# Kernel optimization log

Measured on AMD Instinct MI355X. Metric: run time of the kernel, lower is better.

Reference implementation:

```python
import jax, jax.numpy as jnp
import numpy as np

N_NODES = 50000
N_EDGES = 800000
D = 128
H = 8
HD = D // H
N_NTYPES = 3
N_ETYPES = 5
LN_EPS = 1e-5


def setup_inputs() -> dict:
    key = jax.random.key(0)
    ks = jax.random.split(key, 16)
    inp = {
        "x": jax.random.normal(ks[0], (N_NODES, D), dtype=jnp.float32),
        "edge_index": jax.random.randint(ks[1], (2, N_EDGES), 0, N_NODES),
        "edge_type": jax.random.randint(ks[2], (N_EDGES,), 0, N_ETYPES),
        "node_type": jax.random.randint(ks[3], (N_NODES,), 0, N_NTYPES),
        # per-(node_type, head) QKV projections, per-(edge_type, head) K transform
        "W_Q": jax.random.normal(ks[4], (N_NTYPES, H, HD, HD), dtype=jnp.float32) * 0.02,
        "W_K": jax.random.normal(ks[5], (N_NTYPES, H, HD, HD), dtype=jnp.float32) * 0.02,
        "W_V": jax.random.normal(ks[6], (N_NTYPES, H, HD, HD), dtype=jnp.float32) * 0.02,
        "W_edge": jax.random.normal(ks[7], (N_ETYPES, H, HD, HD), dtype=jnp.float32) * 0.02,
        "mu": jnp.ones((H, N_ETYPES), dtype=jnp.float32),
        "W_out": jax.random.normal(ks[8], (D, D), dtype=jnp.float32) * 0.02,
        "b_out": jnp.zeros((D,), dtype=jnp.float32),
        "ln1_g": jnp.ones((D,), dtype=jnp.float32),
        "ln1_b": jnp.zeros((D,), dtype=jnp.float32),
        "W1": jax.random.normal(ks[9], (D, 4 * D), dtype=jnp.float32) * 0.02,
        "b1": jnp.zeros((4 * D,), dtype=jnp.float32),
        "W2": jax.random.normal(ks[10], (4 * D, D), dtype=jnp.float32) * 0.02,
        "b2": jnp.zeros((D,), dtype=jnp.float32),
        "ln2_g": jnp.ones((D,), dtype=jnp.float32),
        "ln2_b": jnp.zeros((D,), dtype=jnp.float32),
    }
    return inp


def _layer_norm(y, g, b):
    m = y.mean(-1, keepdims=True)
    v = ((y - m) ** 2).mean(-1, keepdims=True)
    return (y - m) * jax.lax.rsqrt(v + LN_EPS) * g + b


def reference(x, edge_index, edge_type, node_type,
              W_Q, W_K, W_V, W_edge, mu,
              W_out, b_out, ln1_g, ln1_b, W1, b1, W2, b2, ln2_g, ln2_b):
    N = x.shape[0]
    xh = x.reshape(N, H, HD)  # heads vectorized (concat of per-head slices)

    # type-specific QKV: small fixed loop over node types, masked select
    Q = jnp.zeros_like(xh)
    K = jnp.zeros_like(xh)
    V = jnp.zeros_like(xh)
    for t in range(N_NTYPES):
        m = (node_type == t)[:, None, None]
        Q = jnp.where(m, jnp.einsum('nhd,hdf->nhf', xh, W_Q[t]), Q)
        K = jnp.where(m, jnp.einsum('nhd,hdf->nhf', xh, W_K[t]), K)
        V = jnp.where(m, jnp.einsum('nhd,hdf->nhf', xh, W_V[t]), V)

    src, dst = edge_index[0], edge_index[1]
    q_dst = Q[dst]   # [E,H,HD]
    k_src = K[src]   # [E,H,HD]

    # edge-type-specific K transform
    kt = jnp.zeros_like(k_src)
    for et in range(N_ETYPES):
        m = (edge_type == et)[:, None, None]
        kt = jnp.where(m, jnp.einsum('ehd,hdf->ehf', k_src, W_edge[et]), kt)

    scores = (q_dst * kt).sum(-1) / jnp.sqrt(jnp.float32(HD))  # [E,H]
    scores = scores * mu[:, edge_type].T                       # mu per edge type, per head

    # sparse softmax over incoming edges of each dst node, per head
    smax = jax.ops.segment_max(scores, dst, num_segments=N)
    ex = jnp.exp(scores - smax[dst])
    den = jax.ops.segment_sum(ex, dst, num_segments=N)
    w = ex / (den[dst] + 1e-10)                                 # [E,H]

    agg = jax.ops.segment_sum(V[src] * w[..., None], dst, num_segments=N)  # [N,H,HD]
    mh = agg.reshape(N, D) @ W_out + b_out  # dropout is identity in eval

    h = _layer_norm(x + mh, ln1_g, ln1_b)
    ffn = jax.nn.gelu(h @ W1 + b1, approximate=False) @ W2 + b2
    return _layer_norm(h + ffn, ln2_g, ln2_b)
```

## Files before the change

### kernel.cpp

```cpp
#include <hip/hip_runtime.h>
#include <hip/hip_bf16.h>

#define N_NODESC 50000
#define N_EDGESC 800000
#define DD 128
#define HH 8
#define HDIM 16
#define N_NT 3
#define N_ET 5
#define NPB 196
#define NEB 400
#define NFB 512
#define WPB 912

#define KV8_OFF    ((size_t)0)
#define QT8_OFF    ((size_t)12800000)
#define AGG_OFF    ((size_t)57600000)
#define WOUTT_OFF  ((size_t)83200000)
#define W1T_OFF    ((size_t)83232768)
#define W2T_OFF    ((size_t)83363840)
#define WHPF_OFF   ((size_t)83494912)
#define EDATA_OFF  ((size_t)84183040)
#define ROWS_OFF   ((size_t)87383040)
#define ORIG_OFF   ((size_t)87583104)
#define DEG_OFF    ((size_t)87783104)
#define TOFS_OFF   ((size_t)87983104)
#define BH_OFF     ((size_t)87983168)
#define BB_OFF     ((size_t)87985536)
#define TMP_OFF    ((size_t)87988928)
#define RLOC_OFF   ((size_t)91188928)
#define CSUM_OFF   ((size_t)91389056)

using short8 = __attribute__((ext_vector_type(8))) short;
using f32x4  = __attribute__((ext_vector_type(4))) float;
using f32x2  = __attribute__((ext_vector_type(2))) float;

__device__ __forceinline__ ushort f2b(float f) {
    __hip_bfloat16 h = __float2bfloat16(f);
    return *(ushort*)&h;
}
__device__ __forceinline__ float b2f(ushort u) {
    __hip_bfloat16 h = *(__hip_bfloat16*)&u;
    return __bfloat162float(h);
}
__device__ __forceinline__ f32x2 pk0(unsigned int w) {
    return __builtin_amdgcn_cvt_pk_f32_fp8((int)w, false);
}
__device__ __forceinline__ f32x2 pk1(unsigned int w) {
    return __builtin_amdgcn_cvt_pk_f32_fp8((int)w, true);
}
__device__ __forceinline__ float gelu_f(float v) {
    const float x = v * 0.70710678118654752f;
    const float ax = fabsf(x);
    const float d = fmaf(0.3275911f, ax, 1.0f);
    float t;
    asm("v_rcp_f32 %0, %1" : "=v"(t) : "v"(d));
    float p = fmaf(1.061405429f, t, -1.453152027f);
    p = fmaf(p, t, 1.421413741f);
    p = fmaf(p, t, -0.284496736f);
    p = fmaf(p, t, 0.254829592f);
    p = p * t;
    const float e = __expf(-ax * ax);
    const float er = 1.0f - p * e;
    const float erfx = (x < 0.f) ? -er : er;
    return 0.5f * v * (1.0f + erfx);
}
__device__ __forceinline__ void ebar() {
    __builtin_amdgcn_sched_barrier(0);
    asm volatile("s_waitcnt lgkmcnt(0)" ::: "memory");
    __builtin_amdgcn_sched_barrier(0);
    __builtin_amdgcn_s_barrier();
    __builtin_amdgcn_sched_barrier(0);
}

__global__ __launch_bounds__(256) void prep_a(
    const float* __restrict__ Wout, const float* __restrict__ W1, const float* __restrict__ W2,
    const float* __restrict__ WQ, const float* __restrict__ Wk, const float* __restrict__ Wv,
    const float* __restrict__ We, const float* __restrict__ mu,
    ushort* __restrict__ Woutt, ushort* __restrict__ W1t, ushort* __restrict__ W2t,
    ushort* __restrict__ Whpf,
    const int* __restrict__ ntype, int* __restrict__ bh,
    const int* __restrict__ dst, int* __restrict__ deg, unsigned int* __restrict__ tmp)
{
    const int b = blockIdx.x, tid = threadIdx.x;
    if (b < WPB) {
        const int gid = b * 256 + tid;
        if (gid < 16384) {
            const int nn = gid >> 7, k = gid & 127;
            Woutt[gid] = f2b(Wout[k * 128 + nn]);
        } else if (gid < 81920) {
            const int i = gid - 16384;
            const int nn = i >> 7, k = i & 127;
            W1t[i] = f2b(W1[k * 512 + nn]);
        } else if (gid < 147456) {
            const int i = gid - 81920;
            const int nn = i >> 9, k = i & 511;
            W2t[i] = f2b(W2[k * 128 + nn]);
        } else {
            const int idx = gid - 147456;
            const int t = idx / 28672;
            const int r = idx % 28672;
            const int i = r & 7;
            const int l = (r >> 3) & 63;
            const int f = r >> 9;
            const int j = f % 14, p = f / 14;
            const int c = j * 16 + (l & 15);
            const int k = ((l >> 4) << 3) + i;
            const int hi = (c >= 112) ? 1 : 0;
            const int h = 2 * p + hi;
            float v = 0.f;
            if ((k >> 4) == hi) {
                const int kp = k & 15;
                const int cl = c - hi * 112;
                if (cl < 16) {
                    v = 4.f * Wk[((t * HH + h) * HDIM + kp) * HDIM + cl];
                } else if (cl < 32) {
                    v = 4.f * Wv[((t * HH + h) * HDIM + kp) * HDIM + (cl - 16)];
                } else {
                    const int et = (cl - 32) >> 4, jj = (cl - 32) & 15;
                    const float* wq = WQ + ((t * HH + h) * HDIM + kp) * HDIM;
                    const float* we = We + ((et * HH + h) * HDIM + jj) * HDIM;
                    float s = 0.f;
#pragma unroll
                    for (int ff = 0; ff < 16; ff++) s = fmaf(wq[ff], we[ff], s);
                    v = 64.f * mu[h * N_ET + et] * s;
                }
            }
            Whpf[idx] = f2b(v);
        }
    } else if (b < WPB + NPB) {
        const int bc = b - WPB;
        const int wave = tid >> 6, lane = tid & 63;
        const int n = bc * 256 + tid;
        const int t = (n < N_NODESC) ? ntype[n] : -1;
        const unsigned long long m0 = __ballot(t == 0);
        const unsigned long long m1 = __ballot(t == 1);
        const unsigned long long m2 = __ballot(t == 2);
        __shared__ int wcnt[4][3];
        if (lane == 0) {
            wcnt[wave][0] = (int)__popcll(m0);
            wcnt[wave][1] = (int)__popcll(m1);
            wcnt[wave][2] = (int)__popcll(m2);
        }
        __syncthreads();
        if (tid < 3)
            bh[tid * NPB + bc] = wcnt[0][tid] + wcnt[1][tid] + wcnt[2][tid] + wcnt[3][tid];
    } else {
        for (int e = (b - WPB - NPB) * 256 + tid; e < N_EDGESC; e += NEB * 256) {
            const int nd = dst[e];
            const unsigned int p = (unsigned int)atomicAdd(&deg[nd], 1);
            tmp[e] = (p << 16) | (unsigned int)nd;
        }
    }
}

__global__ __launch_bounds__(256) void prep_b(
    const int* __restrict__ bh, const int* __restrict__ deg,
    int* __restrict__ bb, int* __restrict__ tofs,
    int* __restrict__ rloc, int* __restrict__ csum)
{
    __shared__ int part[256];
    const int tid = threadIdx.x;
    if (blockIdx.x == 0) {
        const int base3 = tid * 3;
        int e0 = (base3 + 0 < 588) ? bh[base3 + 0] : 0;
        int e1 = (base3 + 1 < 588) ? bh[base3 + 1] : 0;
        int e2 = (base3 + 2 < 588) ? bh[base3 + 2] : 0;
        const int l0 = e0, l1 = e0 + e1, l2 = l1 + e2;
        part[tid] = l2;
        __syncthreads();
        for (int off = 1; off < 256; off <<= 1) {
            const int u = (tid >= off) ? part[tid - off] : 0;
            __syncthreads();
            part[tid] += u;
            __syncthreads();
        }
        const int tb = part[tid] - l2;
        if (base3 + 0 < 588) bb[base3 + 0] = tb;
        if (base3 + 1 < 588) bb[base3 + 1] = tb + l0;
        if (base3 + 2 < 588) bb[base3 + 2] = tb + l1;
        __syncthreads();
        if (tid == 0) {
            tofs[0] = 0;
            tofs[1] = bb[NPB];
            tofs[2] = bb[2 * NPB];
            tofs[3] = N_NODESC;
        }
    } else {
        const int c = blockIdx.x - 1;
        const int n = c * 256 + tid;
        const int vdeg = (n < N_NODESC) ? deg[n] : 0;
        part[tid] = vdeg;
        __syncthreads();
        for (int off = 1; off < 256; off <<= 1) {
            const int u = (tid >= off) ? part[tid - off] : 0;
            __syncthreads();
            part[tid] += u;
            __syncthreads();
        }
        if (n <= N_NODESC) rloc[n] = part[tid] - vdeg;
        if (tid == 255) csum[c] = part[255];
    }
}

__global__ __launch_bounds__(256) void prep_c(
    const int* __restrict__ ntype,
    const int* __restrict__ src, const int* __restrict__ etype,
    const int* __restrict__ bb, const int* __restrict__ rloc, const int* __restrict__ csum,
    const unsigned int* __restrict__ tmp,
    int* __restrict__ origof, int* __restrict__ rows,
    int* __restrict__ edata)
{
    const int b = blockIdx.x, tid = threadIdx.x;
    __shared__ int cb[256];
    {
        const int v = (tid < NPB) ? csum[tid] : 0;
        cb[tid] = v;
        __syncthreads();
        for (int off = 1; off < 256; off <<= 1) {
            const int u = (tid >= off) ? cb[tid - off] : 0;
            __syncthreads();
            cb[tid] += u;
            __syncthreads();
        }
        const int incl = cb[tid];
        __syncthreads();
        cb[tid] = incl - v;
        __syncthreads();
    }

    if (b < NPB) {
        const int wave = tid >> 6, lane = tid & 63;
        const int n = b * 256 + tid;
        const int t = (n < N_NODESC) ? ntype[n] : -1;
        const unsigned long long m0 = __ballot(t == 0);
        const unsigned long long m1 = __ballot(t == 1);
        const unsigned long long m2 = __ballot(t == 2);
        __shared__ int wcnt[4][3];
        if (lane == 0) {
            wcnt[wave][0] = (int)__popcll(m0);
            wcnt[wave][1] = (int)__popcll(m1);
            wcnt[wave][2] = (int)__popcll(m2);
        }
        __syncthreads();
        if (n < N_NODESC) {
            int basew = 0;
#pragma unroll
            for (int w = 0; w < 4; w++) if (w < wave) basew += wcnt[w][t];
            const unsigned long long mt = (t == 0) ? m0 : (t == 1) ? m1 : m2;
            const unsigned long long mlt = ((unsigned long long)1 << lane) - 1;
            const int p = bb[t * NPB + b] + basew + (int)__popcll(mt & mlt);
            origof[p] = n;
        }
        if (n <= N_NODESC) rows[n] = cb[b] + rloc[n];
    } else {
        for (int e = (b - NPB) * 256 + tid; e < N_EDGESC; e += NFB * 256) {
            const unsigned int v = tmp[e];
            const int nd = (int)(v & 0xffffu);
            const int p = (int)(v >> 16);
            edata[cb[nd >> 8] + rloc[nd] + p] = src[e] | (etype[e] << 16);
        }
    }
}

#define LDX 132

__global__ __launch_bounds__(256) void proj_gemm(
    const float* __restrict__ x, const ushort* __restrict__ Whpf,
    const int* __restrict__ tofs, const int* __restrict__ origof,
    unsigned char* __restrict__ KV8b, unsigned char* __restrict__ Qt8)
{
    const int t = blockIdx.y;
    const int rs = tofs[t], re = tofs[t + 1];
    const int mBase = rs + blockIdx.x * 64;
    if (mBase >= re) return;

    __shared__ ushort Xs[64 * LDX];
    __shared__ ushort Ws[28672];

    const int tid = threadIdx.x;
    const int lane = tid & 63, wave = tid >> 6;
    const int l15 = lane & 15, rq = (lane >> 4) * 4;

#pragma unroll
    for (int it = 0; it < 4; it++) {
        const int idx = it * 256 + tid;
        const int row = idx >> 4, ch = idx & 15;
        int gm = mBase + row; if (gm >= N_NODESC) gm = N_NODESC - 1;
        const int og = origof[gm];
        const float4 v0 = *(const float4*)(x + (size_t)og * DD + ch * 8);
        const float4 v1 = *(const float4*)(x + (size_t)og * DD + ch * 8 + 4);
        ushort o[8] = {f2b(v0.x), f2b(v0.y), f2b(v0.z), f2b(v0.w),
                       f2b(v1.x), f2b(v1.y), f2b(v1.z), f2b(v1.w)};
        *(uint4*)&Xs[row * LDX + ch * 8] = *(uint4*)o;
    }
    const ushort* Wg = Whpf + (size_t)t * 28672;
#pragma unroll
    for (int it = 0; it < 14; it++) {
        const int idx = it * 256 + tid;
        *(uint4*)&Ws[idx * 8] = *(const uint4*)(Wg + (size_t)idx * 8);
    }
    __syncthreads();

    int ogr[4]; bool vr[4];
#pragma unroll
    for (int r = 0; r < 4; r++) {
        const int gm = mBase + wave * 16 + rq + r;
        vr[r] = (gm < re);
        ogr[r] = vr[r] ? origof[gm] : 0;
    }

    for (int p = 0; p < 4; p++) {
        const short8 af = *(const short8*)&Xs[(wave * 16 + l15) * LDX + p * 32 + (lane >> 4) * 8];
#pragma unroll
        for (int j = 0; j < 14; j++) {
            const short8 bf = *(const short8*)&Ws[((p * 14 + j) * 64 + lane) * 8];
            f32x4 c = __builtin_amdgcn_mfma_f32_16x16x32_bf16(
                af, bf, (f32x4){0.f, 0.f, 0.f, 0.f}, 0, 0, 0);
            const int hi = (j >= 7) ? 1 : 0;
            const int h = 2 * p + hi;
            const int jj = j - hi * 7;
#pragma unroll
            for (int r = 0; r < 4; r++) {
                if (!vr[r]) continue;
                const float v = c[r];
                const unsigned char b8 =
                    (unsigned char)(__builtin_amdgcn_cvt_pk_fp8_f32(v, v, 0, false) & 0xff);
                const size_t og = (size_t)ogr[r];
                if (jj == 0)      KV8b[og * 256 + h * 16 + l15] = b8;
                else if (jj == 1) KV8b[og * 256 + 128 + h * 16 + l15] = b8;
                else              Qt8[og * 640 + (jj - 2) * 128 + h * 16 + l15] = b8;
            }
        }
    }
}

__global__ __launch_bounds__(128) void edgeagg_kernel(
    const int* __restrict__ rowstart, const int* __restrict__ edata,
    const unsigned char* __restrict__ Qt8, const unsigned char* __restrict__ KV8,
    ushort* __restrict__ agg)
{
    const int w = threadIdx.x >> 6;
    const int lane = threadIdx.x & 63;
    const int n = blockIdx.x * 2 + w;
    const int slot = lane >> 3;
    const int h = lane & 7;

    __shared__ uint4 qs8s[2][40];
    if (lane < 40)
        qs8s[w][lane] = ((const uint4*)(Qt8 + (size_t)n * 640))[lane];
    __syncthreads();
    const uint* qbase = (const uint*)&qs8s[w][0];

    const int s0 = rowstart[n], s1 = rowstart[n + 1];
    const float qsc = 1.44269504f / 1024.f;

    float acc[16];
#pragma unroll
    for (int j = 0; j < 16; j++) acc[j] = 0.f;
    float den = 0.f;

    int i = s0 + slot;
    int ed = 0;
    uint4 kw = {0u, 0u, 0u, 0u}, vw = {0u, 0u, 0u, 0u};
    if (i < s1) {
        ed = edata[i];
        const unsigned char* kvp = KV8 + ((size_t)(ed & 0xffff) << 8);
        kw = *(const uint4*)(kvp + (h << 4));
        vw = *(const uint4*)(kvp + 128 + (h << 4));
    }
    while (i < s1) {
        const int in2 = i + 8;
        int edn = 0;
        uint4 kwn = {0u, 0u, 0u, 0u}, vwn = {0u, 0u, 0u, 0u};
        if (in2 < s1) {
            edn = edata[in2];
            const unsigned char* kvpn = KV8 + ((size_t)(edn & 0xffff) << 8);
            kwn = *(const uint4*)(kvpn + (h << 4));
            vwn = *(const uint4*)(kvpn + 128 + (h << 4));
        }

        const int et = ed >> 16;
        const uint4 qw = *(const uint4*)(qbase + (et << 5) + (h << 2));

        const f32x2 q0 = pk0(qw.x), q1 = pk1(qw.x), q2 = pk0(qw.y), q3 = pk1(qw.y);
        const f32x2 q4 = pk0(qw.z), q5 = pk1(qw.z), q6 = pk0(qw.w), q7 = pk1(qw.w);
        const f32x2 k0 = pk0(kw.x), k1 = pk1(kw.x), k2 = pk0(kw.y), k3 = pk1(kw.y);
        const f32x2 k4 = pk0(kw.z), k5 = pk1(kw.z), k6 = pk0(kw.w), k7 = pk1(kw.w);

        float pa = q0.x * k0.x;
        float pb = q0.y * k0.y;
        float pc = q1.x * k1.x;
        float pd = q1.y * k1.y;
        pa = fmaf(q2.x, k2.x, pa); pb = fmaf(q2.y, k2.y, pb);
        pc = fmaf(q3.x, k3.x, pc); pd = fmaf(q3.y, k3.y, pd);
        pa = fmaf(q4.x, k4.x, pa); pb = fmaf(q4.y, k4.y, pb);
        pc = fmaf(q5.x, k5.x, pc); pd = fmaf(q5.y, k5.y, pd);
        pa = fmaf(q6.x, k6.x, pa); pb = fmaf(q6.y, k6.y, pb);
        pc = fmaf(q7.x, k7.x, pc); pd = fmaf(q7.y, k7.y, pd);

        const float ex = exp2f(((pa + pb) + (pc + pd)) * qsc);
        den += ex;

        const f32x2 v0 = pk0(vw.x), v1 = pk1(vw.x), v2 = pk0(vw.y), v3 = pk1(vw.y);
        const f32x2 v4 = pk0(vw.z), v5 = pk1(vw.z), v6 = pk0(vw.w), v7 = pk1(vw.w);
        acc[0]  = fmaf(ex, v0.x, acc[0]);  acc[1]  = fmaf(ex, v0.y, acc[1]);
        acc[2]  = fmaf(ex, v1.x, acc[2]);  acc[3]  = fmaf(ex, v1.y, acc[3]);
        acc[4]  = fmaf(ex, v2.x, acc[4]);  acc[5]  = fmaf(ex, v2.y, acc[5]);
        acc[6]  = fmaf(ex, v3.x, acc[6]);  acc[7]  = fmaf(ex, v3.y, acc[7]);
        acc[8]  = fmaf(ex, v4.x, acc[8]);  acc[9]  = fmaf(ex, v4.y, acc[9]);
        acc[10] = fmaf(ex, v5.x, acc[10]); acc[11] = fmaf(ex, v5.y, acc[11]);
        acc[12] = fmaf(ex, v6.x, acc[12]); acc[13] = fmaf(ex, v6.y, acc[13]);
        acc[14] = fmaf(ex, v7.x, acc[14]); acc[15] = fmaf(ex, v7.y, acc[15]);

        i = in2; ed = edn; kw = kwn; vw = vwn;
    }

    {
        const int b0 = slot & 1, b1 = slot & 2, b2 = slot & 4;
#pragma unroll
        for (int j = 0; j < 8; j++) {
            const float v = b0 ? acc[j] : acc[j + 8];
            const float r = __shfl_xor(v, 8);
            acc[j] = (b0 ? acc[j + 8] : acc[j]) + r;
        }
#pragma unroll
        for (int j = 0; j < 4; j++) {
            const float v = b1 ? acc[j] : acc[j + 4];
            const float r = __shfl_xor(v, 16);
            acc[j] = (b1 ? acc[j + 4] : acc[j]) + r;
        }
#pragma unroll
        for (int j = 0; j < 2; j++) {
            const float v = b2 ? acc[j] : acc[j + 2];
            const float r = __shfl_xor(v, 32);
            acc[j] = (b2 ? acc[j + 2] : acc[j]) + r;
        }
        den += __shfl_xor(den, 8);
        den += __shfl_xor(den, 16);
        den += __shfl_xor(den, 32);
    }
    const float rr = 0.25f / (den + 1e-10f);
    const int fb = (h << 4) + ((slot & 1) << 3) + ((slot & 2) << 1) + ((slot & 4) >> 1);
    ushort o2[2] = { f2b(acc[0] * rr), f2b(acc[1] * rr) };
    *(uint*)&agg[((size_t)n << 7) + fb] = *(uint*)o2;
}

#define LDH 132
#define LDB2 68

#define LOADB(P0, P1, PTR) { P0 = *(const short8*)(PTR); P1 = *(const short8*)((PTR) + 8); }
#define STAGEB1(P0, P1) { *(short8*)&Bs[br * LDB2 + bc] = P0; \
                          *(short8*)&Bs[br * LDB2 + bc + 8] = P1; }
#define COMP(ASRC, KOFF, ACC) { \
    short8 af[2], bf[2]; \
    _Pragma("unroll") \
    for (int kk2 = 0; kk2 < 2; kk2++) { \
        _Pragma("unroll") \
        for (int i = 0; i < 2; i++) \
            af[i] = *(const short8*)&ASRC[(wm * 32 + i * 16 + l15) * LDH + (KOFF) + kk2 * 32 + q8]; \
        _Pragma("unroll") \
        for (int j = 0; j < 2; j++) \
            bf[j] = *(const short8*)&Bs[(wn * 32 + j * 16 + l15) * LDB2 + kk2 * 32 + q8]; \
        _Pragma("unroll") \
        for (int i = 0; i < 2; i++) \
            _Pragma("unroll") \
            for (int j = 0; j < 2; j++) \
                ACC[i][j] = __builtin_amdgcn_mfma_f32_16x16x32_bf16(af[i], bf[j], ACC[i][j], 0, 0, 0); \
    } }

__global__ __launch_bounds__(512, 4) void fused_tail(
    const ushort* __restrict__ agg, const ushort* __restrict__ Woutt,
    const ushort* __restrict__ W1t, const ushort* __restrict__ W2t,
    const float* __restrict__ x,
    const float* __restrict__ bout, const float* __restrict__ g1, const float* __restrict__ b1ln,
    const float* __restrict__ b1, const float* __restrict__ b2,
    const float* __restrict__ g2, const float* __restrict__ b2ln,
    float* __restrict__ out)
{
    __shared__ ushort Bs[128 * LDB2];
    __shared__ ushort Hs[64 * LDH];
    __shared__ ushort Ts[64 * LDH];
    __shared__ float red[2][4][64];

    const int tid = threadIdx.x;
    const int lane = tid & 63, wave = tid >> 6;
    const int wm = wave >> 2, wn = wave & 3;
    const int l15 = lane & 15, q8 = (lane >> 4) * 8, rq = (lane >> 4) * 4;
    const int mBase = blockIdx.x * 64;

    const int br = tid >> 2, bc = (tid & 3) * 16;
    const int ar = tid >> 3, ac = (tid & 7) * 16;
    int rowA = mBase + ar; if (rowA >= N_NODESC) rowA = N_NODESC - 1;

    f32x4 acc1[2][2], acc2[2][2];
#pragma unroll
    for (int i = 0; i < 2; i++)
#pragma unroll
        for (int j = 0; j < 2; j++) {
            acc1[i][j] = (f32x4){0.f, 0.f, 0.f, 0.f};
            acc2[i][j] = (f32x4){0.f, 0.f, 0.f, 0.f};
        }

    short8 pB0, pB1, aT0, aT1;
    LOADB(pB0, pB1, Woutt + (size_t)br * 128 + bc);
    aT0 = *(const short8*)(agg + (size_t)rowA * DD + ac);
    aT1 = *(const short8*)(agg + (size_t)rowA * DD + ac + 8);
    float xv[2][4][2];
#pragma unroll
    for (int i = 0; i < 2; i++)
#pragma unroll
        for (int r = 0; r < 4; r++) {
            const int gm = mBase + wm * 32 + i * 16 + rq + r;
            const int gr = (gm < N_NODESC) ? gm : N_NODESC - 1;
#pragma unroll
            for (int j = 0; j < 2; j++)
                xv[i][r][j] = x[(size_t)gr * DD + wn * 32 + j * 16 + l15];
        }
    *(short8*)&Ts[ar * LDH + ac] = aT0;
    *(short8*)&Ts[ar * LDH + ac + 8] = aT1;
    STAGEB1(pB0, pB1);
    LOADB(pB0, pB1, Woutt + (size_t)br * 128 + 64 + bc);
    ebar();

    COMP(Ts, 0, acc1);
    ebar();
    STAGEB1(pB0, pB1);
    LOADB(pB0, pB1, W1t + (size_t)br * 128 + bc);
    ebar();
    COMP(Ts, 64, acc1);

    {
        float bo[2], gv[2], bv[2];
#pragma unroll
        for (int j = 0; j < 2; j++) {
            const int gn = wn * 32 + j * 16 + l15;
            bo[j] = bout[gn]; gv[j] = g1[gn]; bv[j] = b1ln[gn];
        }
#pragma unroll
        for (int i = 0; i < 2; i++) {
#pragma unroll
            for (int r = 0; r < 4; r++) {
                const int row = wm * 32 + i * 16 + rq + r;
                float s = 0.f, ss = 0.f;
#pragma unroll
                for (int j = 0; j < 2; j++) {
                    float v = acc1[i][j][r] + bo[j] + xv[i][r][j];
                    acc1[i][j][r] = v;
                    s += v; ss += v * v;
                }
                s  += __shfl_xor(s, 1);  s  += __shfl_xor(s, 2);  s  += __shfl_xor(s, 4);  s  += __shfl_xor(s, 8);
                ss += __shfl_xor(ss, 1); ss += __shfl_xor(ss, 2); ss += __shfl_xor(ss, 4); ss += __shfl_xor(ss, 8);
                if (l15 == 0) { red[0][wn][row] = s; red[1][wn][row] = ss; }
            }
        }
        ebar();
#pragma unroll
        for (int i = 0; i < 2; i++) {
#pragma unroll
            for (int r = 0; r < 4; r++) {
                const int row = wm * 32 + i * 16 + rq + r;
                const float s  = red[0][0][row] + red[0][1][row] + red[0][2][row] + red[0][3][row];
                const float ss = red[1][0][row] + red[1][1][row] + red[1][2][row] + red[1][3][row];
                const float mean = s * (1.f / 128.f);
                const float var  = ss * (1.f / 128.f) - mean * mean;
                const float rstd = rsqrtf(var + 1e-5f);
#pragma unroll
                for (int j = 0; j < 2; j++) {
                    const int gn = wn * 32 + j * 16 + l15;
                    Hs[row * LDH + gn] = f2b((acc1[i][j][r] - mean) * rstd * gv[j] + bv[j]);
                }
            }
        }
    }

    for (int nb = 0; nb < 4; nb++) {
        f32x4 a1[2][2];
#pragma unroll
        for (int i = 0; i < 2; i++)
#pragma unroll
            for (int j = 0; j < 2; j++) a1[i][j] = (f32x4){0.f, 0.f, 0.f, 0.f};

        ebar();
        STAGEB1(pB0, pB1);
        LOADB(pB0, pB1, W1t + (size_t)(nb * 128 + br) * 128 + 64 + bc);
        ebar();
        COMP(Hs, 0, a1);

        ebar();
        STAGEB1(pB0, pB1);
        LOADB(pB0, pB1, W2t + (size_t)br * 512 + nb * 128 + bc);
        ebar();
        COMP(Hs, 64, a1);

        {
            float b1v[2];
#pragma unroll
            for (int j = 0; j < 2; j++)
                b1v[j] = b1[nb * 128 + wn * 32 + j * 16 + l15];
#pragma unroll
            for (int i = 0; i < 2; i++)
#pragma unroll
                for (int j = 0; j < 2; j++)
#pragma unroll
                    for (int r = 0; r < 4; r++) {
                        const int row = wm * 32 + i * 16 + rq + r;
                        const int col = wn * 32 + j * 16 + l15;
                        Ts[row * LDH + col] = f2b(gelu_f(a1[i][j][r] + b1v[j]));
                    }
        }

        ebar();
        STAGEB1(pB0, pB1);
        LOADB(pB0, pB1, W2t + (size_t)br * 512 + nb * 128 + 64 + bc);
        ebar();
        COMP(Ts, 0, acc2);

        ebar();
        STAGEB1(pB0, pB1);
        if (nb < 3) { LOADB(pB0, pB1, W1t + (size_t)((nb + 1) * 128 + br) * 128 + bc); }
        ebar();
        COMP(Ts, 64, acc2);
    }

    {
        float b2v[2], gv[2], bv[2];
#pragma unroll
        for (int j = 0; j < 2; j++) {
            const int gn = wn * 32 + j * 16 + l15;
            b2v[j] = b2[gn]; gv[j] = g2[gn]; bv[j] = b2ln[gn];
        }
#pragma unroll
        for (int i = 0; i < 2; i++) {
#pragma unroll
            for (int r = 0; r < 4; r++) {
                const int row = wm * 32 + i * 16 + rq + r;
                float s = 0.f, ss = 0.f;
#pragma unroll
                for (int j = 0; j < 2; j++) {
                    const int gn = wn * 32 + j * 16 + l15;
                    float v = acc2[i][j][r] + b2v[j] + b2f(Hs[row * LDH + gn]);
                    acc2[i][j][r] = v;
                    s += v; ss += v * v;
                }
                s  += __shfl_xor(s, 1);  s  += __shfl_xor(s, 2);  s  += __shfl_xor(s, 4);  s  += __shfl_xor(s, 8);
                ss += __shfl_xor(ss, 1); ss += __shfl_xor(ss, 2); ss += __shfl_xor(ss, 4); ss += __shfl_xor(ss, 8);
                if (l15 == 0) { red[0][wn][row] = s; red[1][wn][row] = ss; }
            }
        }
        ebar();
#pragma unroll
        for (int i = 0; i < 2; i++) {
#pragma unroll
            for (int r = 0; r < 4; r++) {
                const int row = wm * 32 + i * 16 + rq + r;
                const int gm = mBase + row;
                if (gm >= N_NODESC) continue;
                const float s  = red[0][0][row] + red[0][1][row] + red[0][2][row] + red[0][3][row];
                const float ss = red[1][0][row] + red[1][1][row] + red[1][2][row] + red[1][3][row];
                const float mean = s * (1.f / 128.f);
                const float var  = ss * (1.f / 128.f) - mean * mean;
                const float rstd = rsqrtf(var + 1e-5f);
#pragma unroll
                for (int j = 0; j < 2; j++) {
                    const int gn = wn * 32 + j * 16 + l15;
                    out[(size_t)gm * DD + gn] = (acc2[i][j][r] - mean) * rstd * gv[j] + bv[j];
                }
            }
        }
    }
}

extern "C" void kernel_launch(void* const* d_in, const int* in_sizes, int n_in,
                              void* d_out, int out_size, void* d_ws, size_t ws_size,
                              hipStream_t stream)
{
    const float* x     = (const float*)d_in[0];
    const int*   ei    = (const int*)d_in[1];
    const int*   etyp  = (const int*)d_in[2];
    const int*   ntype = (const int*)d_in[3];
    const float* Wq    = (const float*)d_in[4];
    const float* Wk    = (const float*)d_in[5];
    const float* Wv    = (const float*)d_in[6];
    const float* We    = (const float*)d_in[7];
    const float* mu    = (const float*)d_in[8];
    const float* Wout  = (const float*)d_in[9];
    const float* bout  = (const float*)d_in[10];
    const float* g1    = (const float*)d_in[11];
    const float* b1ln  = (const float*)d_in[12];
    const float* W1    = (const float*)d_in[13];
    const float* b1    = (const float*)d_in[14];
    const float* W2    = (const float*)d_in[15];
    const float* b2    = (const float*)d_in[16];
    const float* g2    = (const float*)d_in[17];
    const float* b2ln  = (const float*)d_in[18];
    float* out = (float*)d_out;

    char* ws = (char*)d_ws;
    ushort*        KV8   = (ushort*)(ws + KV8_OFF);
    unsigned char* Qt8   = (unsigned char*)(ws + QT8_OFF);
    ushort*        agg   = (ushort*)(ws + AGG_OFF);
    ushort*        Woutt = (ushort*)(ws + WOUTT_OFF);
    ushort*        W1t   = (ushort*)(ws + W1T_OFF);
    ushort*        W2t   = (ushort*)(ws + W2T_OFF);
    ushort*        Whpf  = (ushort*)(ws + WHPF_OFF);
    int*           edata = (int*)(ws + EDATA_OFF);
    int*           rows  = (int*)(ws + ROWS_OFF);
    int*           origof= (int*)(ws + ORIG_OFF);
    int*           deg   = (int*)(ws + DEG_OFF);
    int*           tofs  = (int*)(ws + TOFS_OFF);
    int*           bh    = (int*)(ws + BH_OFF);
    int*           bb    = (int*)(ws + BB_OFF);
    unsigned int*  tmp   = (unsigned int*)(ws + TMP_OFF);
    int*           rloc  = (int*)(ws + RLOC_OFF);
    int*           csum  = (int*)(ws + CSUM_OFF);

    const int* srcA = ei;
    const int* dstA = ei + N_EDGESC;

    (void)hipMemsetAsync(ws + DEG_OFF, 0, 200000, stream);

    prep_a<<<WPB + NPB + NEB, 256, 0, stream>>>(
        Wout, W1, W2, Wq, Wk, Wv, We, mu, Woutt, W1t, W2t, Whpf,
        ntype, bh, dstA, deg, tmp);
    prep_b<<<1 + NPB, 256, 0, stream>>>(bh, deg, bb, tofs, rloc, csum);
    prep_c<<<NPB + NFB, 256, 0, stream>>>(ntype, srcA, etyp, bb, rloc, csum, tmp,
                                          origof, rows, edata);

    proj_gemm<<<dim3(782, 3), 256, 0, stream>>>(x, Whpf, tofs, origof,
                                                (unsigned char*)KV8, Qt8);
    edgeagg_kernel<<<N_NODESC / 2, 128, 0, stream>>>(rows, edata, Qt8,
                                                     (const unsigned char*)KV8, agg);

    fused_tail<<<782, 512, 0, stream>>>(agg, Woutt, W1t, W2t, x,
                                        bout, g1, b1ln, b1, b2, g2, b2ln, out);
}
```

Measured before the change: 313.2 us.

## Drop node-type sort; compute per-type projections with masked MFMA passes

```diff
diff --git a/kernel.cpp b/kernel.cpp
--- a/kernel.cpp
+++ b/kernel.cpp
@@ -22,11 +22,7 @@
 #define WHPF_OFF   ((size_t)83494912)
 #define EDATA_OFF  ((size_t)84183040)
 #define ROWS_OFF   ((size_t)87383040)
-#define ORIG_OFF   ((size_t)87583104)
 #define DEG_OFF    ((size_t)87783104)
-#define TOFS_OFF   ((size_t)87983104)
-#define BH_OFF     ((size_t)87983168)
-#define BB_OFF     ((size_t)87985536)
 #define TMP_OFF    ((size_t)87988928)
 #define RLOC_OFF   ((size_t)91188928)
 #define CSUM_OFF   ((size_t)91389056)
@@ -79,7 +75,6 @@
     const float* __restrict__ We, const float* __restrict__ mu,
     ushort* __restrict__ Woutt, ushort* __restrict__ W1t, ushort* __restrict__ W2t,
     ushort* __restrict__ Whpf,
-    const int* __restrict__ ntype, int* __restrict__ bh,
     const int* __restrict__ dst, int* __restrict__ deg, unsigned int* __restrict__ tmp)
 {
     const int b = blockIdx.x, tid = threadIdx.x;
@@ -128,25 +123,8 @@
             }
             Whpf[idx] = f2b(v);
         }
-    } else if (b < WPB + NPB) {
-        const int bc = b - WPB;
-        const int wave = tid >> 6, lane = tid & 63;
-        const int n = bc * 256 + tid;
-        const int t = (n < N_NODESC) ? ntype[n] : -1;
-        const unsigned long long m0 = __ballot(t == 0);
-        const unsigned long long m1 = __ballot(t == 1);
-        const unsigned long long m2 = __ballot(t == 2);
-        __shared__ int wcnt[4][3];
-        if (lane == 0) {
-            wcnt[wave][0] = (int)__popcll(m0);
-            wcnt[wave][1] = (int)__popcll(m1);
-            wcnt[wave][2] = (int)__popcll(m2);
-        }
-        __syncthreads();
-        if (tid < 3)
-            bh[tid * NPB + bc] = wcnt[0][tid] + wcnt[1][tid] + wcnt[2][tid] + wcnt[3][tid];
     } else {
-        for (int e = (b - WPB - NPB) * 256 + tid; e < N_EDGESC; e += NEB * 256) {
+        for (int e = (b - WPB) * 256 + tid; e < N_EDGESC; e += NEB * 256) {
             const int nd = dst[e];
             const unsigned int p = (unsigned int)atomicAdd(&deg[nd], 1);
             tmp[e] = (p << 16) | (unsigned int)nd;
@@ -155,61 +133,31 @@
 }
 
 __global__ __launch_bounds__(256) void prep_b(
-    const int* __restrict__ bh, const int* __restrict__ deg,
-    int* __restrict__ bb, int* __restrict__ tofs,
+    const int* __restrict__ deg,
     int* __restrict__ rloc, int* __restrict__ csum)
 {
     __shared__ int part[256];
     const int tid = threadIdx.x;
-    if (blockIdx.x == 0) {
-        const int base3 = tid * 3;
-        int e0 = (base3 + 0 < 588) ? bh[base3 + 0] : 0;
-        int e1 = (base3 + 1 < 588) ? bh[base3 + 1] : 0;
-        int e2 = (base3 + 2 < 588) ? bh[base3 + 2] : 0;
-        const int l0 = e0, l1 = e0 + e1, l2 = l1 + e2;
-        part[tid] = l2;
+    const int c = blockIdx.x;
+    const int n = c * 256 + tid;
+    const int vdeg = (n < N_NODESC) ? deg[n] : 0;
+    part[tid] = vdeg;
+    __syncthreads();
+    for (int off = 1; off < 256; off <<= 1) {
+        const int u = (tid >= off) ? part[tid - off] : 0;
         __syncthreads();
-        for (int off = 1; off < 256; off <<= 1) {
-            const int u = (tid >= off) ? part[tid - off] : 0;
-            __syncthreads();
-            part[tid] += u;
-            __syncthreads();
-        }
-        const int tb = part[tid] - l2;
-        if (base3 + 0 < 588) bb[base3 + 0] = tb;
-        if (base3 + 1 < 588) bb[base3 + 1] = tb + l0;
-        if (base3 + 2 < 588) bb[base3 + 2] = tb + l1;
+        part[tid] += u;
         __syncthreads();
-        if (tid == 0) {
-            tofs[0] = 0;
-            tofs[1] = bb[NPB];
-            tofs[2] = bb[2 * NPB];
-            tofs[3] = N_NODESC;
-        }
-    } else {
-        const int c = blockIdx.x - 1;
-        const int n = c * 256 + tid;
-        const int vdeg = (n < N_NODESC) ? deg[n] : 0;
-        part[tid] = vdeg;
-        __syncthreads();
-        for (int off = 1; off < 256; off <<= 1) {
-            const int u = (tid >= off) ? part[tid - off] : 0;
-            __syncthreads();
-            part[tid] += u;
-            __syncthreads();
-        }
-        if (n <= N_NODESC) rloc[n] = part[tid] - vdeg;
-        if (tid == 255) csum[c] = part[255];
-    }
+    }
+    if (n <= N_NODESC) rloc[n] = part[tid] - vdeg;
+    if (tid == 255) csum[c] = part[255];
 }
 
 __global__ __launch_bounds__(256) void prep_c(
-    const int* __restrict__ ntype,
     const int* __restrict__ src, const int* __restrict__ etype,
-    const int* __restrict__ bb, const int* __restrict__ rloc, const int* __restrict__ csum,
+    const int* __restrict__ rloc, const int* __restrict__ csum,
     const unsigned int* __restrict__ tmp,
-    int* __restrict__ origof, int* __restrict__ rows,
-    int* __restrict__ edata)
+    int* __restrict__ rows, int* __restrict__ edata)
 {
     const int b = blockIdx.x, tid = threadIdx.x;
     __shared__ int cb[256];
@@ -230,28 +178,7 @@
     }
 
     if (b < NPB) {
-        const int wave = tid >> 6, lane = tid & 63;
         const int n = b * 256 + tid;
-        const int t = (n < N_NODESC) ? ntype[n] : -1;
-        const unsigned long long m0 = __ballot(t == 0);
-        const unsigned long long m1 = __ballot(t == 1);
-        const unsigned long long m2 = __ballot(t == 2);
-        __shared__ int wcnt[4][3];
-        if (lane == 0) {
-            wcnt[wave][0] = (int)__popcll(m0);
-            wcnt[wave][1] = (int)__popcll(m1);
-            wcnt[wave][2] = (int)__popcll(m2);
-        }
-        __syncthreads();
-        if (n < N_NODESC) {
-            int basew = 0;
-#pragma unroll
-            for (int w = 0; w < 4; w++) if (w < wave) basew += wcnt[w][t];
-            const unsigned long long mt = (t == 0) ? m0 : (t == 1) ? m1 : m2;
-            const unsigned long long mlt = ((unsigned long long)1 << lane) - 1;
-            const int p = bb[t * NPB + b] + basew + (int)__popcll(mt & mlt);
-            origof[p] = n;
-        }
         if (n <= N_NODESC) rows[n] = cb[b] + rloc[n];
     } else {
         for (int e = (b - NPB) * 256 + tid; e < N_EDGESC; e += NFB * 256) {
@@ -267,16 +194,13 @@
 
 __global__ __launch_bounds__(256) void proj_gemm(
     const float* __restrict__ x, const ushort* __restrict__ Whpf,
-    const int* __restrict__ tofs, const int* __restrict__ origof,
+    const int* __restrict__ ntype,
     unsigned char* __restrict__ KV8b, unsigned char* __restrict__ Qt8)
 {
-    const int t = blockIdx.y;
-    const int rs = tofs[t], re = tofs[t + 1];
-    const int mBase = rs + blockIdx.x * 64;
-    if (mBase >= re) return;
+    const int mBase = blockIdx.x * 64;
+    if (mBase >= N_NODESC) return;
 
     __shared__ ushort Xs[64 * LDX];
-    __shared__ ushort Ws[28672];
 
     const int tid = threadIdx.x;
     const int lane = tid & 63, wave = tid >> 6;
@@ -286,50 +210,49 @@
     for (int it = 0; it < 4; it++) {
         const int idx = it * 256 + tid;
         const int row = idx >> 4, ch = idx & 15;
-        int gm = mBase + row; if (gm >= N_NODESC) gm = N_NODESC - 1;
-        const int og = origof[gm];
-        const float4 v0 = *(const float4*)(x + (size_t)og * DD + ch * 8);
-        const float4 v1 = *(const float4*)(x + (size_t)og * DD + ch * 8 + 4);
+        int gr = mBase + row; if (gr >= N_NODESC) gr = N_NODESC - 1;
+        const float4 v0 = *(const float4*)(x + (size_t)gr * DD + ch * 8);
+        const float4 v1 = *(const float4*)(x + (size_t)gr * DD + ch * 8 + 4);
         ushort o[8] = {f2b(v0.x), f2b(v0.y), f2b(v0.z), f2b(v0.w),
                        f2b(v1.x), f2b(v1.y), f2b(v1.z), f2b(v1.w)};
         *(uint4*)&Xs[row * LDX + ch * 8] = *(uint4*)o;
     }
-    const ushort* Wg = Whpf + (size_t)t * 28672;
-#pragma unroll
-    for (int it = 0; it < 14; it++) {
-        const int idx = it * 256 + tid;
-        *(uint4*)&Ws[idx * 8] = *(const uint4*)(Wg + (size_t)idx * 8);
-    }
     __syncthreads();
 
-    int ogr[4]; bool vr[4];
+    int trow[4];
 #pragma unroll
     for (int r = 0; r < 4; r++) {
         const int gm = mBase + wave * 16 + rq + r;
-        vr[r] = (gm < re);
-        ogr[r] = vr[r] ? origof[gm] : 0;
-    }
-
-    for (int p = 0; p < 4; p++) {
-        const short8 af = *(const short8*)&Xs[(wave * 16 + l15) * LDX + p * 32 + (lane >> 4) * 8];
-#pragma unroll
-        for (int j = 0; j < 14; j++) {
-            const short8 bf = *(const short8*)&Ws[((p * 14 + j) * 64 + lane) * 8];
-            f32x4 c = __builtin_amdgcn_mfma_f32_16x16x32_bf16(
-                af, bf, (f32x4){0.f, 0.f, 0.f, 0.f}, 0, 0, 0);
-            const int hi = (j >= 7) ? 1 : 0;
-            const int h = 2 * p + hi;
-            const int jj = j - hi * 7;
-#pragma unroll
-            for (int r = 0; r < 4; r++) {
-                if (!vr[r]) continue;
-                const float v = c[r];
-                const unsigned char b8 =
-                    (unsigned char)(__builtin_amdgcn_cvt_pk_fp8_f32(v, v, 0, false) & 0xff);
-                const size_t og = (size_t)ogr[r];
-                if (jj == 0)      KV8b[og * 256 + h * 16 + l15] = b8;
-                else if (jj == 1) KV8b[og * 256 + 128 + h * 16 + l15] = b8;
-                else              Qt8[og * 640 + (jj - 2) * 128 + h * 16 + l15] = b8;
+        trow[r] = (gm < N_NODESC) ? ntype[gm] : -1;
+    }
+
+    for (int t = 0; t < 3; t++) {
+        bool anyl = false;
+#pragma unroll
+        for (int r = 0; r < 4; r++) anyl |= (trow[r] == t);
+        if (!__any((int)anyl)) continue;
+        const ushort* Wg = Whpf + (size_t)t * 28672;
+        for (int p = 0; p < 4; p++) {
+            const short8 af = *(const short8*)&Xs[(wave * 16 + l15) * LDX + p * 32 + (lane >> 4) * 8];
+#pragma unroll
+            for (int j = 0; j < 14; j++) {
+                const short8 bf = *(const short8*)(Wg + ((size_t)(p * 14 + j) * 64 + lane) * 8);
+                f32x4 c = __builtin_amdgcn_mfma_f32_16x16x32_bf16(
+                    af, bf, (f32x4){0.f, 0.f, 0.f, 0.f}, 0, 0, 0);
+                const int hi = (j >= 7) ? 1 : 0;
+                const int h = 2 * p + hi;
+                const int jj = j - hi * 7;
+#pragma unroll
+                for (int r = 0; r < 4; r++) {
+                    if (trow[r] != t) continue;
+                    const size_t og = (size_t)(mBase + wave * 16 + rq + r);
+                    const float v = c[r];
+                    const unsigned char b8 =
+                        (unsigned char)(__builtin_amdgcn_cvt_pk_fp8_f32(v, v, 0, false) & 0xff);
+                    if (jj == 0)      KV8b[og * 256 + h * 16 + l15] = b8;
+                    else if (jj == 1) KV8b[og * 256 + 128 + h * 16 + l15] = b8;
+                    else              Qt8[og * 640 + (jj - 2) * 128 + h * 16 + l15] = b8;
+                }
             }
         }
     }
@@ -706,11 +629,7 @@
     ushort*        Whpf  = (ushort*)(ws + WHPF_OFF);
     int*           edata = (int*)(ws + EDATA_OFF);
     int*           rows  = (int*)(ws + ROWS_OFF);
-    int*           origof= (int*)(ws + ORIG_OFF);
     int*           deg   = (int*)(ws + DEG_OFF);
-    int*           tofs  = (int*)(ws + TOFS_OFF);
-    int*           bh    = (int*)(ws + BH_OFF);
-    int*           bb    = (int*)(ws + BB_OFF);
     unsigned int*  tmp   = (unsigned int*)(ws + TMP_OFF);
     int*           rloc  = (int*)(ws + RLOC_OFF);
     int*           csum  = (int*)(ws + CSUM_OFF);
@@ -720,15 +639,13 @@
 
     (void)hipMemsetAsync(ws + DEG_OFF, 0, 200000, stream);
 
-    prep_a<<<WPB + NPB + NEB, 256, 0, stream>>>(
+    prep_a<<<WPB + NEB, 256, 0, stream>>>(
         Wout, W1, W2, Wq, Wk, Wv, We, mu, Woutt, W1t, W2t, Whpf,
-        ntype, bh, dstA, deg, tmp);
-    prep_b<<<1 + NPB, 256, 0, stream>>>(bh, deg, bb, tofs, rloc, csum);
-    prep_c<<<NPB + NFB, 256, 0, stream>>>(ntype, srcA, etyp, bb, rloc, csum, tmp,
-                                          origof, rows, edata);
-
-    proj_gemm<<<dim3(782, 3), 256, 0, stream>>>(x, Whpf, tofs, origof,
-                                                (unsigned char*)KV8, Qt8);
+        dstA, deg, tmp);
+    prep_b<<<NPB, 256, 0, stream>>>(deg, rloc, csum);
+    prep_c<<<NPB + NFB, 256, 0, stream>>>(srcA, etyp, rloc, csum, tmp, rows, edata);
+
+    proj_gemm<<<782, 256, 0, stream>>>(x, Whpf, ntype, (unsigned char*)KV8, Qt8);
     edgeagg_kernel<<<N_NODESC / 2, 128, 0, stream>>>(rows, edata, Qt8,
                                                      (const unsigned char*)KV8, agg);
 
```

Result: slower. 328.2 us (+4.8%).
